# Optimization experiments

Measured on AMD Instinct MI355X. Metric: run time of the kernel, lower is better.

## Reference

```python
import jax, jax.numpy as jnp
import numpy as np

KS = 3          # kernel_size
DIL = 6         # dilation
PAD = 6         # padding
N = KS * KS     # sampling points per pixel
EPS = 1e-5      # BatchNorm eps


def conv2d(x, w, b=None, padding=0):
    out = jax.lax.conv_general_dilated(
        x, w, window_strides=(1, 1),
        padding=[(padding, padding), (padding, padding)],
        dimension_numbers=('NCHW', 'OIHW', 'NCHW'))
    if b is not None:
        out = out + b[None, :, None, None]
    return out


def setup_inputs() -> dict:
    key = jax.random.key(0)
    ks = jax.random.split(key, 6)
    B, C, H, W, P = 4, 256, 64, 64, 256
    x = jax.random.normal(ks[0], (B, C, H, W), jnp.float32)
    # offset-predicting conv (2N channels), kaiming-ish scale, kept small so offsets are sane
    w_p = jax.random.normal(ks[1], (2 * N, C, 3, 3), jnp.float32) * 0.02
    b_p = jnp.zeros((2 * N,), jnp.float32)
    # modulation-mask conv (N channels)
    w_m = jax.random.normal(ks[2], (N, C, 3, 3), jnp.float32) * 0.02
    b_m = jnp.zeros((N,), jnp.float32)
    # main deform-conv weight (no bias)
    w = jax.random.normal(ks[3], (P, C, KS, KS), jnp.float32) * (2.0 / (C * N)) ** 0.5
    gamma = jnp.ones((P,), jnp.float32)   # BN weight (init fill 1)
    beta = jnp.zeros((P,), jnp.float32)   # BN bias  (init fill 0)
    return dict(x=x, w_p=w_p, b_p=b_p, w_m=w_m, b_m=b_m, w=w, gamma=gamma, beta=beta)


def deform_conv(x, w_p, b_p, w_m, b_m, w):
    B, C, H, W = x.shape
    offset = conv2d(x, w_p, b_p, padding=1)                 # [B, 2N, H, W]
    m = jax.nn.sigmoid(conv2d(x, w_m, b_m, padding=1))      # [B, N, H, W] modulation mask

    x_pad = jnp.pad(x, ((0, 0), (0, 0), (PAD, PAD), (PAD, PAD)))
    Hp, Wp = H + 2 * PAD, W + 2 * PAD

    # p = p_0 (base grid, starts at 1 into padded map) + p_n (dilated kernel grid) + offset
    r = (KS - 1) // 2
    pn = jnp.arange(-r, r + 1, dtype=jnp.float32) * DIL
    pn_x, pn_y = jnp.meshgrid(pn, pn, indexing='ij')        # row-major matches conv weight layout
    p0_x = jnp.arange(1, H + 1, dtype=jnp.float32)
    p0_y = jnp.arange(1, W + 1, dtype=jnp.float32)
    off_x = offset[:, :N].transpose(0, 2, 3, 1)             # [B, H, W, N]
    off_y = offset[:, N:].transpose(0, 2, 3, 1)
    px = p0_x[None, :, None, None] + pn_x.reshape(-1)[None, None, None, :] + off_x
    py = p0_y[None, None, :, None] + pn_y.reshape(-1)[None, None, None, :] + off_y

    q_lt_x = jnp.clip(jnp.floor(px), 0, Hp - 1)
    q_lt_y = jnp.clip(jnp.floor(py), 0, Wp - 1)
    q_rb_x = jnp.clip(jnp.floor(px) + 1, 0, Hp - 1)
    q_rb_y = jnp.clip(jnp.floor(py) + 1, 0, Wp - 1)
    px = jnp.clip(px, 0, Hp - 1)
    py = jnp.clip(py, 0, Wp - 1)

    x_flat = x_pad.reshape(B, C, Hp * Wp)

    def gather(qx, qy):
        idx = (qx * Wp + qy).astype(jnp.int32).reshape(B, 1, -1)   # [B,1,H*W*N]
        v = jnp.take_along_axis(x_flat, jnp.broadcast_to(idx, (B, C, idx.shape[-1])), axis=2)
        return v.reshape(B, C, H, W, N)

    # bilinear weights (deform-conv-v2 formulation)
    g_lt = (1 + (q_lt_x - px)) * (1 + (q_lt_y - py))
    g_rb = (1 - (q_rb_x - px)) * (1 - (q_rb_y - py))
    g_lb = (1 + (q_lt_x - px)) * (1 - (q_rb_y - py))
    g_rt = (1 - (q_rb_x - px)) * (1 + (q_lt_y - py))

    x_off = (g_lt[:, None] * gather(q_lt_x, q_lt_y)
             + g_rb[:, None] * gather(q_rb_x, q_rb_y)
             + g_lb[:, None] * gather(q_lt_x, q_rb_y)
             + g_rt[:, None] * gather(q_rb_x, q_lt_y))     # [B, C, H, W, N]

    x_off = x_off * m.transpose(0, 2, 3, 1)[:, None]        # apply modulation

    # stride-KS conv over the tiled x_offset == einsum over kernel positions
    wk = w.reshape(w.shape[0], C, N)
    return jnp.einsum('bchwk,ock->bohw', x_off, wk)


def reference(x, w_p, b_p, w_m, b_m, w, gamma, beta):
    y = deform_conv(x, w_p, b_p, w_m, b_m, w)
    # BatchNorm2d, training mode (batch stats, biased variance)
    mean = y.mean(axis=(0, 2, 3), keepdims=True)
    var = ((y - mean) ** 2).mean(axis=(0, 2, 3), keepdims=True)
    y = (y - mean) * jax.lax.rsqrt(var + EPS)
    y = y * gamma[None, :, None, None] + beta[None, :, None, None]
    return jax.nn.relu(y)
```

## Files before the change

kernel.cpp:

```cpp
#include <hip/hip_runtime.h>
#include <hip/hip_bf16.h>
#include <math.h>

#define CC 256
#define PP 256
#define XSTR 296

#define WS_SUM   0ull
#define WS_SUMSQ 256ull
#define WS_YU    512ull
#define WS_XT    2097664ull
#define WS_WF    4194816ull
#define WS_WPMF  4489728ull

typedef __attribute__((ext_vector_type(8))) short bf16x8;
typedef __attribute__((ext_vector_type(4))) float f32x4;

static __device__ inline unsigned short f2bf(float f) {
  unsigned int u = __float_as_uint(f);
  unsigned int r = (u + 0x7FFFu + ((u >> 16) & 1u)) >> 16;
  return (unsigned short)r;
}
static __device__ inline float bf2f(short s) {
  return __uint_as_float(((unsigned)(unsigned short)s) << 16);
}
static __device__ inline unsigned pack_bf2(float a, float b) {
  union { __hip_bfloat162 h2; unsigned u; } cv;
  cv.h2 = __float22bfloat162_rn(float2{a, b});
  return cv.u;
}

__global__ __launch_bounds__(256) void k_prep(const float* __restrict__ x,
                                              const float* __restrict__ w,
                                              const float* __restrict__ w_p,
                                              const float* __restrict__ w_m,
                                              float* __restrict__ ws) {
  int blk = blockIdx.x, t = threadIdx.x;
  if (blk < 1024) {
    __shared__ float sT[64][65];
    int b = blk >> 8, h = (blk >> 2) & 63, c0 = (blk & 3) * 64;
    const float* xs = x + ((size_t)(b * 256 + c0) * 64 + h) * 64;
    int cl = t >> 6, wl = t & 63;
#pragma unroll
    for (int it = 0; it < 16; ++it) {
      int c = cl + it * 4;
      sT[c][wl] = xs[(size_t)c * 4096 + wl];
    }
    __syncthreads();
    unsigned short* xt = (unsigned short*)(ws + WS_XT) +
                         ((size_t)b * 64 + h) * 16384 + c0;
    int c2 = t & 63, w2l = t >> 6;
#pragma unroll
    for (int it = 0; it < 16; ++it) {
      int w2 = w2l + it * 4;
      xt[(size_t)w2 * 256 + c2] = f2bf(sT[c2][w2]);
    }
  } else {
    int gid = (blk - 1024) * 256 + t;
    if (blk == 1024 && t < 512) ws[WS_SUM + t] = 0.f;
    unsigned short* wfb = (unsigned short*)(ws + WS_WF);
    for (int e = gid; e < 589824; e += 163840) {
      int j = e & 7, ocin = (e >> 3) & 15, quad = (e >> 7) & 3;
      int ot = (e >> 9) & 15, ksg = e >> 13;
      int kb = ksg / 9, ks = ksg - kb * 9;
      int c = kb * 32 + quad * 8 + j;
      int oc = ot * 16 + ocin;
      wfb[e] = f2bf(w[((size_t)oc * CC + c) * 9 + ks]);
    }
    unsigned short* wpmf = (unsigned short*)(ws + WS_WPMF);
    for (int e = gid; e < 73728; e += 163840) {
      int j = e & 7, ocin = (e >> 3) & 15, quad = (e >> 7) & 3;
      int ot = (e >> 9) & 1, ksg = e >> 10;
      int kb = ksg / 9, ks = ksg - kb * 9;
      int c = kb * 32 + quad * 8 + j;
      int oc = ot * 16 + ocin;
      float v = 0.f;
      if (oc < 18)      v = w_p[((size_t)oc * CC + c) * 9 + ks];
      else if (oc < 27) v = w_m[((size_t)(oc - 18) * CC + c) * 9 + ks];
      wpmf[e] = f2bf(v);
    }
  }
}

__global__ __launch_bounds__(512, 6) void k_deform(const float* __restrict__ b_p,
                                                   const float* __restrict__ b_m,
                                                   float* __restrict__ ws) {
  const unsigned short* xT = (const unsigned short*)(ws + WS_XT);
  const unsigned short* wfb = (const unsigned short*)(ws + WS_WF);
  const unsigned short* wpmf = (const unsigned short*)(ws + WS_WPMF);
  unsigned short* y = (unsigned short*)(ws + WS_YU);

  __shared__ __align__(16) unsigned short sXu0[32 * XSTR];
  __shared__ __align__(16) unsigned short sXu1[32 * XSTR];
  __shared__ float sOff[27 * 32];
  __shared__ __align__(16) uint4 sPK[288];

  int t = threadIdx.x, blk = blockIdx.x;
  int xcd = blk & 7, ii = blk >> 3;
  int b = xcd >> 1, h = (xcd & 1) * 32 + (ii >> 1), side = ii & 1;

  int lane = t & 63, wv = __builtin_amdgcn_readfirstlane(t >> 6);
  int q = t & 3, uq = t >> 2;
  const unsigned short* xb = xT + (size_t)b * 1048576;

  {
    int oa[3], odst[3];
#pragma unroll
    for (int r = 0; r < 3; ++r) {
      int u = r * 128 + uq;
      odst[r] = -1;
      oa[r] = -1;
      if (u < 288) {
        int j = u >> 5, px = u & 31;
        int row = h + j / 3 - 1, col = side * 32 + px + j % 3 - 1;
        odst[r] = px * XSTR + j * 32 + q * 8;
        if ((unsigned)row < 64u && (unsigned)col < 64u)
          oa[r] = (row * 64 + col) * 256 + q * 8;
      }
    }
    auto stage1 = [&](int kb, unsigned short* buf) {
      int cb = kb * 32;
#pragma unroll
      for (int r = 0; r < 3; ++r) {
        if (odst[r] >= 0) {
          bf16x8 v = {0, 0, 0, 0, 0, 0, 0, 0};
          if (oa[r] >= 0) v = *(const bf16x8*)(xb + oa[r] + cb);
          *(bf16x8*)&buf[odst[r]] = v;
        }
      }
    };

    int pxt = wv & 1, ot = (wv >> 1) & 1, kh = wv >> 2;
    f32x4 accP = {0.f, 0.f, 0.f, 0.f};
    stage1(0, sXu0);
    __syncthreads();
    for (int kb = 0; kb < 8; ++kb) {
      unsigned short* cur = (kb & 1) ? sXu1 : sXu0;
      unsigned short* nxt = (kb & 1) ? sXu0 : sXu1;
      if (kb < 7) stage1(kb + 1, nxt);
      const unsigned short* bb =
          &cur[(pxt * 16 + (lane & 15)) * XSTR + (lane >> 4) * 8];
#pragma unroll
      for (int ks = 0; ks < 9; ++ks) {
        if ((int)(ks >= 5) == kh) {
          int ksg = kb * 9 + ks;
          bf16x8 af =
              *(const bf16x8*)(wpmf + (size_t)ksg * 1024 + ot * 512 + lane * 8);
          bf16x8 bf = *(const bf16x8*)(bb + ks * 32);
          accP = __builtin_amdgcn_mfma_f32_16x16x32_bf16(af, bf, accP, 0, 0, 0);
        }
      }
      __syncthreads();
    }
    float* sR = (float*)sXu0;
    if (kh == 1) {
      int base = (pxt * 2 + ot) * 256 + lane * 4;
#pragma unroll
      for (int r = 0; r < 4; ++r) sR[base + r] = accP[r];
    }
    __syncthreads();
    if (kh == 0) {
      int base = (pxt * 2 + ot) * 256 + lane * 4;
      int pxl = pxt * 16 + (lane & 15);
#pragma unroll
      for (int r = 0; r < 4; ++r) {
        int oc = ot * 16 + (lane >> 4) * 4 + r;
        if (oc < 27) {
          float v = accP[r] + sR[base + r];
          v += (oc < 18) ? b_p[oc] : b_m[oc - 18];
          if (oc >= 18) v = 1.f / (1.f + expf(-v));
          sOff[oc * 32 + pxl] = v;
        }
      }
    }
    __syncthreads();
  }

  if (t < 288) {
    int k = t >> 5, px = t & 31;
    int w = side * 32 + px;
    float offx = sOff[k * 32 + px];
    float offy = sOff[(9 + k) * 32 + px];
    float mk   = sOff[(18 + k) * 32 + px];
    float pnx = (float)((k / 3 - 1) * 6);
    float pny = (float)((k % 3 - 1) * 6);
    float pxf = (float)(h + 1) + pnx + offx;
    float pyf = (float)(w + 1) + pny + offy;
    float fx = floorf(pxf), fy = floorf(pyf);
    float q0x = fminf(fmaxf(fx, 0.f), 75.f);
    float q1x = fminf(fmaxf(fx + 1.f, 0.f), 75.f);
    float q0y = fminf(fmaxf(fy, 0.f), 75.f);
    float q1y = fminf(fmaxf(fy + 1.f, 0.f), 75.f);
    float pxc = fminf(fmaxf(pxf, 0.f), 75.f);
    float pyc = fminf(fmaxf(pyf, 0.f), 75.f);
    float glt = (1.f + (q0x - pxc)) * (1.f + (q0y - pyc));
    float grb = (1.f - (q1x - pxc)) * (1.f - (q1y - pyc));
    float glb = (1.f + (q0x - pxc)) * (1.f - (q1y - pyc));
    float grt = (1.f - (q1x - pxc)) * (1.f + (q0y - pyc));
    int ix0 = (int)q0x - 6, ix1 = (int)q1x - 6;
    int iy0 = (int)q0y - 6, iy1 = (int)q1y - 6;
    bool v00 = (unsigned)ix0 < 64u && (unsigned)iy0 < 64u;
    bool v11 = (unsigned)ix1 < 64u && (unsigned)iy1 < 64u;
    bool v01 = (unsigned)ix0 < 64u && (unsigned)iy1 < 64u;
    bool v10 = (unsigned)ix1 < 64u && (unsigned)iy0 < 64u;
    uint4 pk;
    pk.x = (v00 ? (unsigned)(ix0 * 64 + iy0) : 0u) |
           ((v11 ? (unsigned)(ix1 * 64 + iy1) : 0u) << 16);
    pk.y = (v01 ? (unsigned)(ix0 * 64 + iy1) : 0u) |
           ((v10 ? (unsigned)(ix1 * 64 + iy0) : 0u) << 16);
    pk.z = (unsigned)f2bf(v00 ? glt * mk : 0.f) |
           ((unsigned)f2bf(v11 ? grb * mk : 0.f) << 16);
    pk.w = (unsigned)f2bf(v01 ? glb * mk : 0.f) |
           ((unsigned)f2bf(v10 ? grt * mk : 0.f) << 16);
    sPK[t] = pk;
  }
  __syncthreads();

  f32x4 acc[2][2];
#pragma unroll
  for (int i = 0; i < 2; ++i)
#pragma unroll
    for (int jj = 0; jj < 2; ++jj) acc[i][jj] = (f32x4){0.f, 0.f, 0.f, 0.f};

  int q8 = q * 8;
  auto stage2 = [&](int kb, unsigned short* buf) {
    int cq = kb * 32 + q8;
#pragma unroll
    for (int r = 0; r < 3; ++r) {
      int u = r * 128 + uq;
      if (u < 288) {
        uint4 pk = sPK[u];
        bf16x8 t0 = *(const bf16x8*)(xb + (int)(pk.x & 0xFFFFu) * 256 + cq);
        bf16x8 t1 = *(const bf16x8*)(xb + (int)(pk.x >> 16) * 256 + cq);
        bf16x8 t2 = *(const bf16x8*)(xb + (int)(pk.y & 0xFFFFu) * 256 + cq);
        bf16x8 t3 = *(const bf16x8*)(xb + (int)(pk.y >> 16) * 256 + cq);
        float g0 = __uint_as_float((pk.z & 0xFFFFu) << 16);
        float g1 = __uint_as_float(pk.z & 0xFFFF0000u);
        float g2 = __uint_as_float((pk.w & 0xFFFFu) << 16);
        float g3 = __uint_as_float(pk.w & 0xFFFF0000u);
        float v[8];
#pragma unroll
        for (int i = 0; i < 8; ++i) {
          float val = g0 * bf2f(t0[i]);
          val = fmaf(g1, bf2f(t1[i]), val);
          val = fmaf(g2, bf2f(t2[i]), val);
          val = fmaf(g3, bf2f(t3[i]), val);
          v[i] = val;
        }
        uint4 w4;
        w4.x = pack_bf2(v[0], v[1]);
        w4.y = pack_bf2(v[2], v[3]);
        w4.z = pack_bf2(v[4], v[5]);
        w4.w = pack_bf2(v[6], v[7]);
        int k = u >> 5, px = u & 31;
        *(uint4*)&buf[px * XSTR + k * 32 + q8] = w4;
      }
    }
  };

  stage2(0, sXu0);
  __syncthreads();
  for (int kb = 0; kb < 8; ++kb) {
    unsigned short* cur = (kb & 1) ? sXu1 : sXu0;
    unsigned short* nxt = (kb & 1) ? sXu0 : sXu1;
    if (kb < 7) stage2(kb + 1, nxt);
    const unsigned short* bb0 = &cur[(lane & 15) * XSTR + (lane >> 4) * 8];
    const unsigned short* bb1 = bb0 + 16 * XSTR;
#pragma unroll
    for (int ks = 0; ks < 9; ++ks) {
      int ksg = kb * 9 + ks;
      const unsigned short* ap =
          wfb + (size_t)ksg * 8192 + (size_t)wv * 1024 + lane * 8;
      bf16x8 af0 = *(const bf16x8*)ap;
      bf16x8 af1 = *(const bf16x8*)(ap + 512);
      bf16x8 bf0 = *(const bf16x8*)(bb0 + ks * 32);
      bf16x8 bf1 = *(const bf16x8*)(bb1 + ks * 32);
      acc[0][0] = __builtin_amdgcn_mfma_f32_16x16x32_bf16(af0, bf0, acc[0][0], 0, 0, 0);
      acc[0][1] = __builtin_amdgcn_mfma_f32_16x16x32_bf16(af0, bf1, acc[0][1], 0, 0, 0);
      acc[1][0] = __builtin_amdgcn_mfma_f32_16x16x32_bf16(af1, bf0, acc[1][0], 0, 0, 0);
      acc[1][1] = __builtin_amdgcn_mfma_f32_16x16x32_bf16(af1, bf1, acc[1][1], 0, 0, 0);
    }
    __syncthreads();
  }

  float* sP = (float*)sXu0;
  float* sP2 = sP + 256;
  int quad = lane >> 4, li = lane & 15;
  size_t ybase = ((size_t)b * PP) * 4096 + h * 64 + side * 32;
#pragma unroll
  for (int otl = 0; otl < 2; ++otl) {
#pragma unroll
    for (int r = 0; r < 4; ++r) {
      int oc = wv * 32 + otl * 16 + quad * 4 + r;
      float v0 = acc[otl][0][r];
      float v1 = acc[otl][1][r];
      unsigned short* yp = y + ybase + (size_t)oc * 4096 + li;
      yp[0] = f2bf(v0);
      yp[16] = f2bf(v1);
      float s = v0 + v1;
      float s2 = fmaf(v0, v0, v1 * v1);
      s += __shfl_xor(s, 1);  s2 += __shfl_xor(s2, 1);
      s += __shfl_xor(s, 2);  s2 += __shfl_xor(s2, 2);
      s += __shfl_xor(s, 4);  s2 += __shfl_xor(s2, 4);
      s += __shfl_xor(s, 8);  s2 += __shfl_xor(s2, 8);
      if (li == 0) {
        sP[oc] = s;
        sP2[oc] = s2;
      }
    }
  }
  __syncthreads();
  if (t < 256) {
    atomicAdd(&ws[WS_SUM + t], sP[t]);
    atomicAdd(&ws[WS_SUMSQ + t], sP2[t]);
  }
}

__global__ __launch_bounds__(256) void k_bnrelu(const float* __restrict__ ws,
                                                const float* __restrict__ gamma,
                                                const float* __restrict__ beta,
                                                float* __restrict__ out) {
  const uint4* y8 = (const uint4*)(ws + WS_YU);
  float4* o4 = (float4*)out;
  const int n8 = 4 * PP * 512;
  for (int i = blockIdx.x * blockDim.x + threadIdx.x; i < n8;
       i += gridDim.x * blockDim.x) {
    int oc = (i >> 9) & 255;
    float s = ws[WS_SUM + oc], s2 = ws[WS_SUMSQ + oc];
    float mean = s * (1.f / 16384.f);
    float var = fmaf(s2, 1.f / 16384.f, -mean * mean);
    float rstd = rsqrtf(var + 1e-5f);
    float sc = gamma[oc] * rstd;
    float sh = fmaf(-mean, sc, beta[oc]);
    uint4 v = y8[i];
    float4 r0, r1;
    r0.x = fmaxf(fmaf(bf2f((short)(v.x & 0xFFFFu)), sc, sh), 0.f);
    r0.y = fmaxf(fmaf(bf2f((short)(v.x >> 16)), sc, sh), 0.f);
    r0.z = fmaxf(fmaf(bf2f((short)(v.y & 0xFFFFu)), sc, sh), 0.f);
    r0.w = fmaxf(fmaf(bf2f((short)(v.y >> 16)), sc, sh), 0.f);
    r1.x = fmaxf(fmaf(bf2f((short)(v.z & 0xFFFFu)), sc, sh), 0.f);
    r1.y = fmaxf(fmaf(bf2f((short)(v.z >> 16)), sc, sh), 0.f);
    r1.z = fmaxf(fmaf(bf2f((short)(v.w & 0xFFFFu)), sc, sh), 0.f);
    r1.w = fmaxf(fmaf(bf2f((short)(v.w >> 16)), sc, sh), 0.f);
    o4[i * 2] = r0;
    o4[i * 2 + 1] = r1;
  }
}

extern "C" void kernel_launch(void* const* d_in, const int* in_sizes, int n_in,
                              void* d_out, int out_size, void* d_ws,
                              size_t ws_size, hipStream_t stream) {
  const float* x     = (const float*)d_in[0];
  const float* w_p   = (const float*)d_in[1];
  const float* b_p   = (const float*)d_in[2];
  const float* w_m   = (const float*)d_in[3];
  const float* b_m   = (const float*)d_in[4];
  const float* w     = (const float*)d_in[5];
  const float* gamma = (const float*)d_in[6];
  const float* beta  = (const float*)d_in[7];
  float* ws  = (float*)d_ws;
  float* out = (float*)d_out;

  k_prep<<<1664, 256, 0, stream>>>(x, w, w_p, w_m, ws);
  k_deform<<<512, 512, 0, stream>>>(b_p, b_m, ws);
  k_bnrelu<<<1024, 256, 0, stream>>>(ws, gamma, beta, out);
}
```

Before: 154.5 us.

## Halve deform-conv pixel tile to 16 and double grid for occupancy

Each block of k_deform now covers 16 output pixels instead of 32, and the grid doubles to 1024 blocks. The offset-conv stage splits its kernel positions over four wave groups instead of two, with a three-way shared-memory reduction. Shared memory per block halves and launch bounds rise to 8 blocks per CU, aiming for more resident waves to hide gather latency. In exchange each weight fragment loaded from global memory now feeds only half as many MFMAs, so weight traffic per output doubles and more per-block atomics and syncs are issued.

```diff
diff --git a/kernel.cpp b/kernel.cpp
--- a/kernel.cpp
+++ b/kernel.cpp
@@ -82,7 +82,7 @@
   }
 }
 
-__global__ __launch_bounds__(512, 6) void k_deform(const float* __restrict__ b_p,
+__global__ __launch_bounds__(512, 8) void k_deform(const float* __restrict__ b_p,
                                                    const float* __restrict__ b_m,
                                                    float* __restrict__ ws) {
   const unsigned short* xT = (const unsigned short*)(ws + WS_XT);
@@ -90,29 +90,31 @@
   const unsigned short* wpmf = (const unsigned short*)(ws + WS_WPMF);
   unsigned short* y = (unsigned short*)(ws + WS_YU);
 
-  __shared__ __align__(16) unsigned short sXu0[32 * XSTR];
-  __shared__ __align__(16) unsigned short sXu1[32 * XSTR];
-  __shared__ float sOff[27 * 32];
-  __shared__ __align__(16) uint4 sPK[288];
+  __shared__ __align__(16) unsigned short sXu0[16 * XSTR];
+  __shared__ __align__(16) unsigned short sXu1[16 * XSTR];
+  __shared__ float sOff[27 * 16];
+  __shared__ __align__(16) uint4 sPK[144];
 
   int t = threadIdx.x, blk = blockIdx.x;
   int xcd = blk & 7, ii = blk >> 3;
-  int b = xcd >> 1, h = (xcd & 1) * 32 + (ii >> 1), side = ii & 1;
+  int b = xcd >> 1;
+  int h = (xcd & 1) * 32 + (ii >> 2);
+  int w0 = ((ii >> 1) & 1) * 32 + (ii & 1) * 16;
 
   int lane = t & 63, wv = __builtin_amdgcn_readfirstlane(t >> 6);
   int q = t & 3, uq = t >> 2;
   const unsigned short* xb = xT + (size_t)b * 1048576;
 
   {
-    int oa[3], odst[3];
-#pragma unroll
-    for (int r = 0; r < 3; ++r) {
+    int oa[2], odst[2];
+#pragma unroll
+    for (int r = 0; r < 2; ++r) {
       int u = r * 128 + uq;
       odst[r] = -1;
       oa[r] = -1;
-      if (u < 288) {
-        int j = u >> 5, px = u & 31;
-        int row = h + j / 3 - 1, col = side * 32 + px + j % 3 - 1;
+      if (u < 144) {
+        int j = u >> 4, px = u & 15;
+        int row = h + j / 3 - 1, col = w0 + px + j % 3 - 1;
         odst[r] = px * XSTR + j * 32 + q * 8;
         if ((unsigned)row < 64u && (unsigned)col < 64u)
           oa[r] = (row * 64 + col) * 256 + q * 8;
@@ -121,7 +123,7 @@
     auto stage1 = [&](int kb, unsigned short* buf) {
       int cb = kb * 32;
 #pragma unroll
-      for (int r = 0; r < 3; ++r) {
+      for (int r = 0; r < 2; ++r) {
         if (odst[r] >= 0) {
           bf16x8 v = {0, 0, 0, 0, 0, 0, 0, 0};
           if (oa[r] >= 0) v = *(const bf16x8*)(xb + oa[r] + cb);
@@ -130,7 +132,7 @@
       }
     };
 
-    int pxt = wv & 1, ot = (wv >> 1) & 1, kh = wv >> 2;
+    int ot = wv & 1, kh = wv >> 1;
     f32x4 accP = {0.f, 0.f, 0.f, 0.f};
     stage1(0, sXu0);
     __syncthreads();
@@ -138,11 +140,11 @@
       unsigned short* cur = (kb & 1) ? sXu1 : sXu0;
       unsigned short* nxt = (kb & 1) ? sXu0 : sXu1;
       if (kb < 7) stage1(kb + 1, nxt);
-      const unsigned short* bb =
-          &cur[(pxt * 16 + (lane & 15)) * XSTR + (lane >> 4) * 8];
+      const unsigned short* bb = &cur[(lane & 15) * XSTR + (lane >> 4) * 8];
 #pragma unroll
       for (int ks = 0; ks < 9; ++ks) {
-        if ((int)(ks >= 5) == kh) {
+        int ksq = (ks < 3) ? 0 : (ks < 5) ? 1 : (ks < 7) ? 2 : 3;
+        if (ksq == kh) {
           int ksg = kb * 9 + ks;
           bf16x8 af =
               *(const bf16x8*)(wpmf + (size_t)ksg * 1024 + ot * 512 + lane * 8);
@@ -153,35 +155,36 @@
       __syncthreads();
     }
     float* sR = (float*)sXu0;
-    if (kh == 1) {
-      int base = (pxt * 2 + ot) * 256 + lane * 4;
+    if (kh != 0) {
+      int base = ((kh - 1) * 2 + ot) * 256 + lane * 4;
 #pragma unroll
       for (int r = 0; r < 4; ++r) sR[base + r] = accP[r];
     }
     __syncthreads();
     if (kh == 0) {
-      int base = (pxt * 2 + ot) * 256 + lane * 4;
-      int pxl = pxt * 16 + (lane & 15);
+      int base = ot * 256 + lane * 4;
+      int pxl = lane & 15;
 #pragma unroll
       for (int r = 0; r < 4; ++r) {
         int oc = ot * 16 + (lane >> 4) * 4 + r;
         if (oc < 27) {
-          float v = accP[r] + sR[base + r];
+          float v = accP[r] + sR[base + r] + sR[512 + base + r] +
+                    sR[1024 + base + r];
           v += (oc < 18) ? b_p[oc] : b_m[oc - 18];
           if (oc >= 18) v = 1.f / (1.f + expf(-v));
-          sOff[oc * 32 + pxl] = v;
+          sOff[oc * 16 + pxl] = v;
         }
       }
     }
     __syncthreads();
   }
 
-  if (t < 288) {
-    int k = t >> 5, px = t & 31;
-    int w = side * 32 + px;
-    float offx = sOff[k * 32 + px];
-    float offy = sOff[(9 + k) * 32 + px];
-    float mk   = sOff[(18 + k) * 32 + px];
+  if (t < 144) {
+    int k = t >> 4, px = t & 15;
+    int w = w0 + px;
+    float offx = sOff[k * 16 + px];
+    float offy = sOff[(9 + k) * 16 + px];
+    float mk   = sOff[(18 + k) * 16 + px];
     float pnx = (float)((k / 3 - 1) * 6);
     float pny = (float)((k % 3 - 1) * 6);
     float pxf = (float)(h + 1) + pnx + offx;
@@ -216,19 +219,17 @@
   }
   __syncthreads();
 
-  f32x4 acc[2][2];
-#pragma unroll
-  for (int i = 0; i < 2; ++i)
-#pragma unroll
-    for (int jj = 0; jj < 2; ++jj) acc[i][jj] = (f32x4){0.f, 0.f, 0.f, 0.f};
+  f32x4 acc[2];
+#pragma unroll
+  for (int i = 0; i < 2; ++i) acc[i] = (f32x4){0.f, 0.f, 0.f, 0.f};
 
   int q8 = q * 8;
   auto stage2 = [&](int kb, unsigned short* buf) {
     int cq = kb * 32 + q8;
 #pragma unroll
-    for (int r = 0; r < 3; ++r) {
+    for (int r = 0; r < 2; ++r) {
       int u = r * 128 + uq;
-      if (u < 288) {
+      if (u < 144) {
         uint4 pk = sPK[u];
         bf16x8 t0 = *(const bf16x8*)(xb + (int)(pk.x & 0xFFFFu) * 256 + cq);
         bf16x8 t1 = *(const bf16x8*)(xb + (int)(pk.x >> 16) * 256 + cq);
@@ -252,7 +253,7 @@
         w4.y = pack_bf2(v[2], v[3]);
         w4.z = pack_bf2(v[4], v[5]);
         w4.w = pack_bf2(v[6], v[7]);
-        int k = u >> 5, px = u & 31;
+        int k = u >> 4, px = u & 15;
         *(uint4*)&buf[px * XSTR + k * 32 + q8] = w4;
       }
     }
@@ -264,8 +265,7 @@
     unsigned short* cur = (kb & 1) ? sXu1 : sXu0;
     unsigned short* nxt = (kb & 1) ? sXu0 : sXu1;
     if (kb < 7) stage2(kb + 1, nxt);
-    const unsigned short* bb0 = &cur[(lane & 15) * XSTR + (lane >> 4) * 8];
-    const unsigned short* bb1 = bb0 + 16 * XSTR;
+    const unsigned short* bb = &cur[(lane & 15) * XSTR + (lane >> 4) * 8];
 #pragma unroll
     for (int ks = 0; ks < 9; ++ks) {
       int ksg = kb * 9 + ks;
@@ -273,12 +273,9 @@
           wfb + (size_t)ksg * 8192 + (size_t)wv * 1024 + lane * 8;
       bf16x8 af0 = *(const bf16x8*)ap;
       bf16x8 af1 = *(const bf16x8*)(ap + 512);
-      bf16x8 bf0 = *(const bf16x8*)(bb0 + ks * 32);
-      bf16x8 bf1 = *(const bf16x8*)(bb1 + ks * 32);
-      acc[0][0] = __builtin_amdgcn_mfma_f32_16x16x32_bf16(af0, bf0, acc[0][0], 0, 0, 0);
-      acc[0][1] = __builtin_amdgcn_mfma_f32_16x16x32_bf16(af0, bf1, acc[0][1], 0, 0, 0);
-      acc[1][0] = __builtin_amdgcn_mfma_f32_16x16x32_bf16(af1, bf0, acc[1][0], 0, 0, 0);
-      acc[1][1] = __builtin_amdgcn_mfma_f32_16x16x32_bf16(af1, bf1, acc[1][1], 0, 0, 0);
+      bf16x8 bf = *(const bf16x8*)(bb + ks * 32);
+      acc[0] = __builtin_amdgcn_mfma_f32_16x16x32_bf16(af0, bf, acc[0], 0, 0, 0);
+      acc[1] = __builtin_amdgcn_mfma_f32_16x16x32_bf16(af1, bf, acc[1], 0, 0, 0);
     }
     __syncthreads();
   }
@@ -286,19 +283,16 @@
   float* sP = (float*)sXu0;
   float* sP2 = sP + 256;
   int quad = lane >> 4, li = lane & 15;
-  size_t ybase = ((size_t)b * PP) * 4096 + h * 64 + side * 32;
+  size_t ybase = ((size_t)b * PP) * 4096 + h * 64 + w0;
 #pragma unroll
   for (int otl = 0; otl < 2; ++otl) {
 #pragma unroll
     for (int r = 0; r < 4; ++r) {
-      int oc = wv * 32 + otl * 16 + quad * 4 + r;
-      float v0 = acc[otl][0][r];
-      float v1 = acc[otl][1][r];
-      unsigned short* yp = y + ybase + (size_t)oc * 4096 + li;
-      yp[0] = f2bf(v0);
-      yp[16] = f2bf(v1);
-      float s = v0 + v1;
-      float s2 = fmaf(v0, v0, v1 * v1);
+      int oc = (wv * 2 + otl) * 16 + quad * 4 + r;
+      float v0 = acc[otl][r];
+      y[ybase + (size_t)oc * 4096 + li] = f2bf(v0);
+      float s = v0;
+      float s2 = v0 * v0;
       s += __shfl_xor(s, 1);  s2 += __shfl_xor(s2, 1);
       s += __shfl_xor(s, 2);  s2 += __shfl_xor(s2, 2);
       s += __shfl_xor(s, 4);  s2 += __shfl_xor(s2, 4);
@@ -362,6 +356,6 @@
   float* out = (float*)d_out;
 
   k_prep<<<1664, 256, 0, stream>>>(x, w, w_p, w_m, ws);
-  k_deform<<<512, 512, 0, stream>>>(b_p, b_m, ws);
+  k_deform<<<1024, 512, 0, stream>>>(b_p, b_m, ws);
   k_bnrelu<<<1024, 256, 0, stream>>>(ws, gamma, beta, out);
 }
```

Measured after the change: 174.7 us. +13.1%, slower.
